# Performance work log

Measured on AMD Instinct MI355X. Metric: run time of the kernel, lower is better.

Reference implementation:

```python
import jax, jax.numpy as jnp
import numpy as np

B, T, DIM = 2, 2048, 2048
H, HKV = 16, 4
D = DIM // H          # head_dim = 128
G = H // HKV          # GQA group = 4
ROPE_BASE = 10000.0
TRAIN_SEQ_LEN = 1024  # Rotary default; T > this triggers NTK base rescale


def _rope_tables():
    # Faithful to Rotary.forward: NTK scaling when seq_len > train_seq_len.
    if T > TRAIN_SEQ_LEN:
        sc = T / TRAIN_SEQ_LEN
        base = ROPE_BASE * sc ** (D / (D - 2))
    else:
        base = ROPE_BASE
    inv = 1.0 / base ** (np.arange(0, D, 2, dtype=np.float32) / D)  # [D/2]
    f = np.outer(np.arange(T, dtype=np.float32), inv)               # [T, D/2]
    cos = jnp.asarray(np.cos(f), jnp.float32)[None, :, None, :]     # [1,T,1,D/2]
    sin = jnp.asarray(np.sin(f), jnp.float32)[None, :, None, :]
    return cos, sin


def _rms_norm(x):
    # F.rms_norm with no weight: x / sqrt(mean(x^2) + eps), eps = finfo(dtype).eps
    eps = jnp.finfo(x.dtype).eps
    return x * jax.lax.rsqrt(jnp.mean(x * x, axis=-1, keepdims=True) + eps)


def _apply_rope(x, cos, sin):
    x1, x2 = jnp.split(x, 2, axis=-1)
    return jnp.concatenate([x1 * cos + x2 * sin, -x1 * sin + x2 * cos], axis=-1)


def setup_inputs() -> dict:
    key = jax.random.key(0)
    kx, kq, kk, kv, kp = jax.random.split(key, 5)
    s = lambda fan_in: 1.0 / np.sqrt(fan_in)
    kv_dim = HKV * D
    return {
        "x": jax.random.normal(kx, (B, T, DIM), jnp.float32),
        "Wq": jax.random.normal(kq, (DIM, DIM), jnp.float32) * s(DIM),
        "Wk": jax.random.normal(kk, (kv_dim, DIM), jnp.float32) * s(DIM),
        "Wv": jax.random.normal(kv, (kv_dim, DIM), jnp.float32) * s(DIM),
        "Wproj": jax.random.normal(kp, (DIM, DIM), jnp.float32) * s(DIM),
        "q_gain": jnp.full((H,), 1.0, jnp.float32),
    }


def reference(x, Wq, Wk, Wv, Wproj, q_gain):
    # QKV projections (bias-free linears)
    q = (x @ Wq.T).reshape(B, T, H, D)
    k = (x @ Wk.T).reshape(B, T, HKV, D)
    v = (x @ Wv.T).reshape(B, T, HKV, D)

    # QK RMSNorm + RoPE + per-head q gain
    q = _rms_norm(q)
    k = _rms_norm(k)
    cos, sin = _rope_tables()
    q = _apply_rope(q, cos, sin)
    k = _apply_rope(k, cos, sin)
    q = q * q_gain[None, None, :, None]

    # GQA causal SDPA without materializing repeated K/V:
    # group query heads by kv head: q -> [B,T,HKV,G,D]
    qg = q.reshape(B, T, HKV, G, D)
    scores = jnp.einsum('btkgd,bskd->bkgts', qg, k) / np.sqrt(D)  # [B,HKV,G,T,T]
    causal = jnp.tril(jnp.ones((T, T), bool))
    scores = jnp.where(causal[None, None, None], scores, -jnp.inf)
    p = jax.nn.softmax(scores, axis=-1)
    y = jnp.einsum('bkgts,bskd->btkgd', p, v).reshape(B, T, H, D)

    out = y.reshape(B, T, DIM) @ Wproj.T
    return out, v
```

## Files before the change

kernel.cpp:

```cpp
#include <hip/hip_runtime.h>
#include <hip/hip_bf16.h>

typedef __bf16 bf16_t;
typedef __bf16 bf16x4 __attribute__((ext_vector_type(4)));
typedef __bf16 bf16x8 __attribute__((ext_vector_type(8)));
typedef float f32x4 __attribute__((ext_vector_type(4)));

#define B_    2
#define T_    2048
#define DIM_  2048
#define H_    16
#define HKV_  4
#define D_    128
#define KVDIM_ 512

__device__ __forceinline__ bf16x8 cvt8(f32x4 a, f32x4 b) {
  bf16x8 r;
  r[0] = (bf16_t)a[0]; r[1] = (bf16_t)a[1]; r[2] = (bf16_t)a[2]; r[3] = (bf16_t)a[3];
  r[4] = (bf16_t)b[0]; r[5] = (bf16_t)b[1]; r[6] = (bf16_t)b[2]; r[7] = (bf16_t)b[3];
  return r;
}
__device__ __forceinline__ bf16x4 cvt4(f32x4 a) {
  bf16x4 r;
  r[0] = (bf16_t)a[0]; r[1] = (bf16_t)a[1]; r[2] = (bf16_t)a[2]; r[3] = (bf16_t)a[3];
  return r;
}
__device__ __forceinline__ void g2l16(const void* g, void* l) {
  __builtin_amdgcn_global_load_lds(
      (const __attribute__((address_space(1))) unsigned int*)g,
      (__attribute__((address_space(3))) unsigned int*)l, 16, 0, 0);
}

__global__ __launch_bounds__(256)
void cvt_all(const float* __restrict__ x,  const float* __restrict__ wq,
             const float* __restrict__ wk, const float* __restrict__ wv,
             const float* __restrict__ wp, bf16_t* __restrict__ xb,
             bf16_t* __restrict__ wqkvb, bf16_t* __restrict__ wpb) {
  int blk = blockIdx.x;
  const float* s; bf16_t* d; int lb;
  if (blk < 4096)      { s = x;  d = xb;                              lb = blk; }
  else if (blk < 6144) { s = wq; d = wqkvb;                           lb = blk - 4096; }
  else if (blk < 6656) { s = wk; d = wqkvb + (size_t)2048 * DIM_;     lb = blk - 6144; }
  else if (blk < 7168) { s = wv; d = wqkvb + (size_t)2560 * DIM_;     lb = blk - 6656; }
  else                 { s = wp; d = wpb;                             lb = blk - 7168; }
  size_t i = (size_t)lb * 2048 + (size_t)threadIdx.x * 8;
  f32x4 a = *(const f32x4*)(s + i);
  f32x4 b = *(const f32x4*)(s + i + 4);
  *(bf16x8*)(d + i) = cvt8(a, b);
}

template <int MODE, bool AASYNC, bool WASYNC>
__global__ __launch_bounds__(256)
void gemm128(const void* __restrict__ Ag, const void* __restrict__ Wg,
             const void* __restrict__ Wg2, void* __restrict__ Cb,
             bf16_t* __restrict__ Kb, bf16_t* __restrict__ Vb,
             float* __restrict__ Vf, int M, int N, int K) {
  constexpr int LDA = AASYNC ? 32 : 40;
  constexpr int LDW = WASYNC ? 32 : 40;
  __shared__ bf16_t As[128 * LDA];
  __shared__ bf16_t Ws[128 * LDW];
  const int tid  = threadIdx.x;
  const int wave = tid >> 6, lane = tid & 63;
  const int l16  = lane & 15, lg = lane >> 4;
  const int m0 = blockIdx.y * 128, n0 = blockIdx.x * 128;
  const int wm = (wave & 1) * 64, wn = (wave >> 1) * 64;
  f32x4 acc[4][4] = {};

  for (int k0 = 0; k0 < K; k0 += 32) {
    __syncthreads();
    if constexpr (AASYNC) {
      const bf16_t* A = (const bf16_t*)Ag;
      const int r = lane >> 2, c8 = (lane & 3) * 8;
      g2l16(&A[(size_t)(m0 + wave * 32 + r) * K + k0 + c8],      &As[(wave * 32) * LDA]);
      g2l16(&A[(size_t)(m0 + wave * 32 + 16 + r) * K + k0 + c8], &As[(wave * 32 + 16) * LDA]);
    } else {
      const float* A = (const float*)Ag;
#pragma unroll
      for (int j = 0; j < 4; j++) {
        int row = wave * 32 + j * 8 + (lane >> 3);
        int cf  = (lane & 7) * 4;
        f32x4 v = *(const f32x4*)&A[(size_t)(m0 + row) * K + k0 + cf];
        *(bf16x4*)&As[row * LDA + cf] = cvt4(v);
      }
    }
    if constexpr (WASYNC) {
      const bf16_t* W = (const bf16_t*)Wg;
      const int r = lane >> 2, c8 = (lane & 3) * 8;
      g2l16(&W[(size_t)(n0 + wave * 32 + r) * K + k0 + c8],      &Ws[(wave * 32) * LDW]);
      g2l16(&W[(size_t)(n0 + wave * 32 + 16 + r) * K + k0 + c8], &Ws[(wave * 32 + 16) * LDW]);
    } else {
      const float* W;
      int nb;
      if constexpr (MODE == 3) {
        if (n0 < 512) { W = (const float*)Wg;  nb = n0; }
        else          { W = (const float*)Wg2; nb = n0 - 512; }
      } else { W = (const float*)Wg; nb = n0; }
#pragma unroll
      for (int j = 0; j < 4; j++) {
        int row = wave * 32 + j * 8 + (lane >> 3);
        int cf  = (lane & 7) * 4;
        f32x4 v = *(const f32x4*)&W[(size_t)(nb + row) * K + k0 + cf];
        *(bf16x4*)&Ws[row * LDW + cf] = cvt4(v);
      }
    }
    __syncthreads();
    bf16x8 af[4], bfr[4];
#pragma unroll
    for (int i = 0; i < 4; i++)
      af[i] = *(const bf16x8*)&As[(wm + i * 16 + l16) * LDA + lg * 8];
#pragma unroll
    for (int j = 0; j < 4; j++)
      bfr[j] = *(const bf16x8*)&Ws[(wn + j * 16 + l16) * LDW + lg * 8];
#pragma unroll
    for (int i = 0; i < 4; i++)
#pragma unroll
      for (int j = 0; j < 4; j++)
        acc[i][j] = __builtin_amdgcn_mfma_f32_16x16x32_bf16(af[i], bfr[j], acc[i][j], 0, 0, 0);
  }
#pragma unroll
  for (int i = 0; i < 4; i++)
#pragma unroll
    for (int j = 0; j < 4; j++) {
      int row = m0 + wm + i * 16 + lg * 4;
      int col = n0 + wn + j * 16 + l16;
#pragma unroll
      for (int r = 0; r < 4; r++) {
        float v = acc[i][j][r];
        if constexpr (MODE == 0) {
          ((bf16_t*)Cb)[(size_t)(row + r) * N + col] = (bf16_t)v;
        } else if constexpr (MODE == 2) {
          ((float*)Cb)[(size_t)(row + r) * N + col] = v;
        } else if constexpr (MODE == 1) {
          if (col < 2048)      ((bf16_t*)Cb)[(size_t)(row + r) * 2048 + col] = (bf16_t)v;
          else if (col < 2560) Kb[(size_t)(row + r) * 512 + (col - 2048)] = (bf16_t)v;
          else {
            int c = col - 2560;
            Vb[(size_t)(row + r) * 512 + c] = (bf16_t)v;
            Vf[(size_t)(row + r) * 512 + c] = v;
          }
        } else {
          if (col < 512) ((bf16_t*)Cb)[(size_t)(row + r) * 512 + col] = (bf16_t)v;
          else {
            int c = col - 512;
            Vb[(size_t)(row + r) * 512 + c] = (bf16_t)v;
            Vf[(size_t)(row + r) * 512 + c] = v;
          }
        }
      }
    }
}

#define SB() __builtin_amdgcn_sched_barrier(0)
#define BARRIER() __builtin_amdgcn_s_barrier()
#define LGKM0() do { asm volatile("s_waitcnt lgkmcnt(0)" ::: "memory"); SB(); } while (0)
#define VMW(N) do { asm volatile("s_waitcnt vmcnt(" #N ")" ::: "memory"); SB(); } while (0)

#define RD_A(BUF, QM) do { \
  _Pragma("unroll") for (int f_ = 0; f_ < 4; f_++) { \
    const int r_ = wm * 128 + (QM) * 64 + f_ * 16 + l16; \
    _Pragma("unroll") for (int ks_ = 0; ks_ < 2; ks_++) \
      a[f_][ks_] = *(const bf16x8*)(lds + (BUF) * 65536 + r_ * 128 + ((ks_ * 64 + lg * 16) ^ swz)); \
  } } while (0)

#define RD_B(BUF, QN, BB) do { \
  _Pragma("unroll") for (int n_ = 0; n_ < 2; n_++) { \
    const int r_ = wn * 64 + (QN) * 32 + n_ * 16 + l16; \
    _Pragma("unroll") for (int ks_ = 0; ks_ < 2; ks_++) \
      BB[n_][ks_] = *(const bf16x8*)(lds + (BUF) * 65536 + 32768 + r_ * 128 + ((ks_ * 64 + lg * 16) ^ swz)); \
  } } while (0)

#define MM(QM, QN, BB) do { \
  __builtin_amdgcn_s_setprio(1); \
  _Pragma("unroll") for (int f_ = 0; f_ < 4; f_++) \
    _Pragma("unroll") for (int n_ = 0; n_ < 2; n_++) \
      _Pragma("unroll") for (int ks_ = 0; ks_ < 2; ks_++) \
        acc[(QM) * 4 + f_][(QN) * 2 + n_] = __builtin_amdgcn_mfma_f32_16x16x32_bf16( \
            a[f_][ks_], BB[n_][ks_], acc[(QM) * 4 + f_][(QN) * 2 + n_], 0, 0, 0); \
  __builtin_amdgcn_s_setprio(0); \
  } while (0)

#define K_ITER(KT0, LAST) do { \
  const int kA1_ = ((KT0) + 1) * 64; \
  const int kN2_ = ((KT0) + 2) * 64; \
  const int kN3_ = ((KT0) + 3) * 64; \
   \
  RD_A(0, 0); RD_B(0, 0, b0); \
  stage_half(Ag, m0, kA1_, 65536); \
  asm volatile("s_waitcnt lgkmcnt(8)" ::: "memory"); \
  SB(); BARRIER(); LGKM0(); \
  MM(0, 0, b0); \
  SB(); BARRIER(); \
   \
  RD_B(0, 1, b1); \
  stage_half(Ag, m0 + 128, kA1_, 65536 + 16384); \
  SB(); BARRIER(); LGKM0(); \
  MM(0, 1, b1); \
  SB(); BARRIER(); \
   \
  RD_A(0, 1); \
  if (!(LAST)) stage_half(Wg, n0, kN2_, 32768); \
  SB(); BARRIER(); LGKM0(); \
  MM(1, 0, b0); \
  SB(); BARRIER(); \
   \
  if (!(LAST)) { stage_half(Wg, n0 + 128, kN2_, 32768 + 16384); VMW(4); } \
  else { VMW(0); } \
  SB(); BARRIER(); \
  MM(1, 1, b1); \
  SB(); BARRIER(); \
   \
  RD_A(1, 0); RD_B(1, 0, b0); \
  if (!(LAST)) stage_half(Ag, m0, kN2_, 0); \
  asm volatile("s_waitcnt lgkmcnt(8)" ::: "memory"); \
  SB(); BARRIER(); LGKM0(); \
  MM(0, 0, b0); \
  SB(); BARRIER(); \
   \
  RD_B(1, 1, b1); \
  if (!(LAST)) stage_half(Ag, m0 + 128, kN2_, 16384); \
  SB(); BARRIER(); LGKM0(); \
  MM(0, 1, b1); \
  SB(); BARRIER(); \
   \
  RD_A(1, 1); \
  if (!(LAST)) stage_half(Wg, n0, kN3_, 65536 + 32768); \
  SB(); BARRIER(); LGKM0(); \
  MM(1, 0, b0); \
  SB(); BARRIER(); \
   \
  if (!(LAST)) { stage_half(Wg, n0 + 128, kN3_, 65536 + 32768 + 16384); VMW(4); } \
  SB(); BARRIER(); \
  MM(1, 1, b1); \
  SB(); BARRIER(); \
} while (0)

template <int MODE>
__global__ __launch_bounds__(512, 2)
void gemm256(const bf16_t* __restrict__ Ag, const bf16_t* __restrict__ Wg,
             void* __restrict__ Cb, bf16_t* __restrict__ Kb, bf16_t* __restrict__ Vb,
             float* __restrict__ Vf, int M, int N, int K) {
  (void)M;
  __shared__ __align__(16) char lds[131072];
  const int tid  = threadIdx.x;
  const int wave = tid >> 6, lane = tid & 63;
  const int l16  = lane & 15, lg = lane >> 4;
  const int wm = wave >> 2, wn = wave & 3;
  const int swz = (l16 & 7) << 4;
  const int m0 = blockIdx.y * 256, n0 = blockIdx.x * 256;
  const int srow = lane >> 3;
  const int scol = ((lane & 7) ^ srow) * 8;

  auto stage_half = [&](const bf16_t* __restrict__ X, int xrow, int k0, int ldsoff) {
    const bf16_t* src = X + (size_t)(xrow + wave * 16 + srow) * K + (k0 + scol);
    char* dst = lds + ldsoff + wave * 2048;
    g2l16(src, dst);
    g2l16(src + (size_t)8 * K, dst + 1024);
  };

  f32x4 acc[8][4] = {};
  bf16x8 a[4][2], b0[2][2], b1[2][2];

  stage_half(Ag, m0,        0, 0);
  stage_half(Ag, m0 + 128,  0, 16384);
  stage_half(Wg, n0,        0, 32768);
  stage_half(Wg, n0 + 128,  0, 32768 + 16384);
  stage_half(Wg, n0,       64, 65536 + 32768);
  stage_half(Wg, n0 + 128, 64, 65536 + 32768 + 16384);
  VMW(4);
  BARRIER();

  const int NIT = K >> 7;
  for (int it = 0; it < NIT - 1; ++it) {
    K_ITER(2 * it, 0);
  }
  K_ITER(2 * (NIT - 1), 1);

#pragma unroll
  for (int mf = 0; mf < 8; mf++)
#pragma unroll
    for (int nf = 0; nf < 4; nf++) {
      const int row = m0 + wm * 128 + mf * 16 + lg * 4;
      const int col = n0 + wn * 64 + nf * 16 + l16;
#pragma unroll
      for (int r = 0; r < 4; r++) {
        float v = acc[mf][nf][r];
        if constexpr (MODE == 1) {
          if (col < 2048)      ((bf16_t*)Cb)[(size_t)(row + r) * 2048 + col] = (bf16_t)v;
          else if (col < 2560) Kb[(size_t)(row + r) * 512 + (col - 2048)] = (bf16_t)v;
          else {
            int c = col - 2560;
            Vb[(size_t)(row + r) * 512 + c] = (bf16_t)v;
            Vf[(size_t)(row + r) * 512 + c] = v;
          }
        } else {
          ((float*)Cb)[(size_t)(row + r) * N + col] = v;
        }
      }
    }
}

__global__ __launch_bounds__(256)
void qk_norm_rope(bf16_t* __restrict__ Qp, bf16_t* __restrict__ Kp,
                  const float* __restrict__ gain) {
  const int lane = threadIdx.x & 63;
  int row = blockIdx.x * 4 + (threadIdx.x >> 6);
  bf16_t* Xp; int nh; bool ag;
  const int MQ = B_ * T_ * H_;
  if (row < MQ) { Xp = Qp; nh = H_;  ag = true; }
  else          { Xp = Kp; nh = HKV_; ag = false; row -= MQ; }
  const int h = row % nh;
  const int t = (row / nh) % T_;
  bf16_t* p = Xp + (size_t)row * D_;
  float x0 = (float)p[lane * 2 + 0];
  float x1 = (float)p[lane * 2 + 1];
  float ss = x0 * x0 + x1 * x1;
#pragma unroll
  for (int m = 32; m >= 1; m >>= 1) ss += __shfl_xor(ss, m);
  const float rn = rsqrtf(ss * (1.0f / 128.0f) + 1.1920929e-07f);
  x0 *= rn; x1 *= rn;
  const float y0 = __shfl_xor(x0, 32);
  const float y1 = __shfl_xor(x1, 32);
  const int i0 = (lane & 31) * 2;
  const float kfreq = -0.22349352180347601f;
  float s0, c0, s1, c1;
  float a0 = (float)t * exp2f(kfreq * (float)i0);
  float a1 = (float)t * exp2f(kfreq * (float)(i0 + 1));
  sincosf(a0, &s0, &c0);
  sincosf(a1, &s1, &c1);
  float o0, o1;
  if (lane < 32) { o0 = x0 * c0 + y0 * s0;  o1 = x1 * c1 + y1 * s1; }
  else           { o0 = x0 * c0 - y0 * s0;  o1 = x1 * c1 - y1 * s1; }
  if (ag) { float g = gain[h]; o0 *= g; o1 *= g; }
  p[lane * 2 + 0] = (bf16_t)o0;
  p[lane * 2 + 1] = (bf16_t)o1;
}

#define KLD 136
#define VLD 72

__global__ __launch_bounds__(256, 2)
void flash_attn(const bf16_t* __restrict__ Q, const bf16_t* __restrict__ Kg,
                const bf16_t* __restrict__ V, bf16_t* __restrict__ Y) {
  __shared__ bf16_t Ks[64 * KLD];
  __shared__ bf16_t Vs[D_ * VLD];
  const int tid  = threadIdx.x;
  const int wave = tid >> 6, lane = tid & 63;
  const int l16  = lane & 15, lg = lane >> 4;
  const int b = blockIdx.z, h = blockIdx.y;
  const int pi = blockIdx.x;
  const int hk = h >> 2;

  int qr[2];
  qr[0] = 64 * pi + 16 * wave;
  qr[1] = 64 * (31 - pi) + 16 * wave;

  bf16x8 qf[2][4];
#pragma unroll
  for (int mt = 0; mt < 2; mt++)
#pragma unroll
    for (int kk = 0; kk < 4; kk++)
      qf[mt][kk] = *(const bf16x8*)&Q[(((size_t)b * T_ + qr[mt] + l16) * H_ + h) * D_ + kk * 32 + lg * 8];

  f32x4 o[2][8] = {};
  float lsum[2] = {};
  const float C = 0.12752531f;

  const int sr = tid >> 4, sc = (tid & 15) * 8;
  const int sp2 = (tid & 31) * 2;
  const int dvh = (tid >> 5) * 8;
  const int ssl = (sp2 & 3) | (((sp2 >> 4) & 1) << 2) | (((sp2 >> 2) & 1) << 3)
                | (((sp2 >> 3) & 1) << 4) | (sp2 & 32);

  bf16x8 kreg[4];
  bf16x8 vreg[2][2];
  auto pf_load = [&](int k0) {
#pragma unroll
    for (int j = 0; j < 4; j++)
      kreg[j] = *(const bf16x8*)&Kg[(((size_t)b * T_ + k0 + sr + 16 * j) * HKV_ + hk) * D_ + sc];
#pragma unroll
    for (int it = 0; it < 2; it++) {
      const bf16_t* vb = &V[(((size_t)b * T_ + k0 + sp2) * HKV_ + hk) * D_ + dvh + it * 64];
      vreg[it][0] = *(const bf16x8*)vb;
      vreg[it][1] = *(const bf16x8*)(vb + HKV_ * D_);
    }
  };
  auto pf_store = [&]() {
#pragma unroll
    for (int j = 0; j < 4; j++)
      *(bf16x8*)&Ks[(sr + 16 * j) * KLD + sc] = kreg[j];
#pragma unroll
    for (int it = 0; it < 2; it++) {
      int dd = dvh + it * 64;
      const unsigned short* au = (const unsigned short*)&vreg[it][0];
      const unsigned short* bu = (const unsigned short*)&vreg[it][1];
#pragma unroll
      for (int i = 0; i < 8; i++) {
        unsigned int pr = (unsigned int)au[i] | ((unsigned int)bu[i] << 16);
        *(unsigned int*)&Vs[(dd + i) * VLD + ssl] = pr;
      }
    }
  };

  const int nkb = 32 - pi;
  pf_load(0);
  for (int kb = 0; kb < nkb; kb++) {
    const int k0 = kb * 64;
    __syncthreads();
    pf_store();
    __syncthreads();
    if (kb + 1 < nkb) pf_load(k0 + 64);

    const bool act0 = (kb <= pi);

    f32x4 s[2][4] = {};
#pragma unroll
    for (int kk = 0; kk < 4; kk++) {
      bf16x8 kf[4];
#pragma unroll
      for (int f = 0; f < 4; f++)
        kf[f] = *(const bf16x8*)&Ks[(f * 16 + l16) * KLD + kk * 32 + lg * 8];
      if (act0)
#pragma unroll
        for (int f = 0; f < 4; f++)
          s[0][f] = __builtin_amdgcn_mfma_f32_16x16x32_bf16(kf[f], qf[0][kk], s[0][f], 0, 0, 0);
#pragma unroll
      for (int f = 0; f < 4; f++)
        s[1][f] = __builtin_amdgcn_mfma_f32_16x16x32_bf16(kf[f], qf[1][kk], s[1][f], 0, 0, 0);
    }
    bf16x8 pfr[2][2];
#pragma unroll
    for (int mt = 0; mt < 2; mt++) {
      if (mt == 0 && !act0) continue;
      const bool diag = (mt == 0) ? (kb == pi) : (kb == nkb - 1);
      const int myq = qr[mt] + l16;
      if (diag) {
#pragma unroll
        for (int f = 0; f < 4; f++)
#pragma unroll
          for (int r = 0; r < 4; r++) {
            int kg = k0 + f * 16 + lg * 4 + r;
            float p = (kg <= myq) ? exp2f(s[mt][f][r] * C) : 0.0f;
            lsum[mt] += p;
            s[mt][f][r] = p;
          }
      } else {
#pragma unroll
        for (int f = 0; f < 4; f++)
#pragma unroll
          for (int r = 0; r < 4; r++) {
            float p = exp2f(s[mt][f][r] * C);
            lsum[mt] += p;
            s[mt][f][r] = p;
          }
      }
      pfr[mt][0] = cvt8(s[mt][0], s[mt][1]);
      pfr[mt][1] = cvt8(s[mt][2], s[mt][3]);
    }
#pragma unroll
    for (int f = 0; f < 8; f++) {
      bf16x8 v0 = *(const bf16x8*)&Vs[(f * 16 + l16) * VLD + lg * 8];
      bf16x8 v1 = *(const bf16x8*)&Vs[(f * 16 + l16) * VLD + 32 + lg * 8];
      if (act0) {
        o[0][f] = __builtin_amdgcn_mfma_f32_16x16x32_bf16(pfr[0][0], v0, o[0][f], 0, 0, 0);
        o[0][f] = __builtin_amdgcn_mfma_f32_16x16x32_bf16(pfr[0][1], v1, o[0][f], 0, 0, 0);
      }
      o[1][f] = __builtin_amdgcn_mfma_f32_16x16x32_bf16(pfr[1][0], v0, o[1][f], 0, 0, 0);
      o[1][f] = __builtin_amdgcn_mfma_f32_16x16x32_bf16(pfr[1][1], v1, o[1][f], 0, 0, 0);
    }
  }
#pragma unroll
  for (int mt = 0; mt < 2; mt++) {
    float l = lsum[mt];
    l += __shfl_xor(l, 16);
    l += __shfl_xor(l, 32);
    const float inv = 1.0f / l;
    float rlv[4];
#pragma unroll
    for (int r = 0; r < 4; r++) rlv[r] = __shfl(inv, lg * 4 + r);
#pragma unroll
    for (int f = 0; f < 8; f++)
#pragma unroll
      for (int r = 0; r < 4; r++) {
        int t = qr[mt] + lg * 4 + r;
        Y[(((size_t)b * T_ + t) * H_ + h) * D_ + f * 16 + l16] = (bf16_t)(o[mt][f][r] * rlv[r]);
      }
  }
}

extern "C" void kernel_launch(void* const* d_in, const int* in_sizes, int n_in,
                              void* d_out, int out_size, void* d_ws, size_t ws_size,
                              hipStream_t stream) {
  (void)in_sizes; (void)n_in; (void)out_size;
  const float* x     = (const float*)d_in[0];
  const float* Wq    = (const float*)d_in[1];
  const float* Wk    = (const float*)d_in[2];
  const float* Wv    = (const float*)d_in[3];
  const float* Wproj = (const float*)d_in[4];
  const float* qgain = (const float*)d_in[5];

  float* out  = (float*)d_out;
  float* vout = out + (size_t)B_ * T_ * DIM_;

  const size_t M = (size_t)B_ * T_;
  char* ws = (char*)d_ws;
  size_t off = 0;
  auto take = [&](size_t elems) { bf16_t* p = (bf16_t*)(ws + off); off += elems * sizeof(bf16_t); return p; };

  bf16_t* Qp = take(M * DIM_);
  bf16_t* Kp = take(M * KVDIM_);
  bf16_t* Vb = take(M * KVDIM_);

  const size_t cvt_elems = M * DIM_ + (size_t)3072 * DIM_ + (size_t)DIM_ * DIM_;
  const bool fast = (ws_size >= off + cvt_elems * sizeof(bf16_t));

  dim3 blk(256);
  if (fast) {
    bf16_t* xb     = take(M * DIM_);
    bf16_t* Wqkvb  = take((size_t)3072 * DIM_);
    bf16_t* Wpb    = take((size_t)DIM_ * DIM_);

    cvt_all<<<dim3(9216), blk, 0, stream>>>(x, Wq, Wk, Wv, Wproj, xb, Wqkvb, Wpb);

    gemm256<1><<<dim3(3072 / 256, M / 256), dim3(512), 0, stream>>>(
        xb, Wqkvb, Qp, Kp, Vb, vout, (int)M, 3072, DIM_);

    qk_norm_rope<<<dim3((unsigned)((M * H_ + M * HKV_) / 4)), blk, 0, stream>>>(Qp, Kp, qgain);
    flash_attn<<<dim3(16, H_, B_), blk, 0, stream>>>(Qp, Kp, Vb, Qp);

    gemm256<2><<<dim3(DIM_ / 256, M / 256), dim3(512), 0, stream>>>(
        Qp, Wpb, out, nullptr, nullptr, nullptr, (int)M, DIM_, DIM_);
  } else {
    gemm128<0, false, false><<<dim3(DIM_ / 128, M / 128), blk, 0, stream>>>(
        x, Wq, nullptr, Qp, nullptr, nullptr, nullptr, M, DIM_, DIM_);
    gemm128<3, false, false><<<dim3(2 * KVDIM_ / 128, M / 128), blk, 0, stream>>>(
        x, Wk, Wv, Kp, nullptr, Vb, vout, M, 2 * KVDIM_, DIM_);
    qk_norm_rope<<<dim3((unsigned)((M * H_ + M * HKV_) / 4)), blk, 0, stream>>>(Qp, Kp, qgain);
    flash_attn<<<dim3(16, H_, B_), blk, 0, stream>>>(Qp, Kp, Vb, Qp);
    gemm128<2, true, false><<<dim3(DIM_ / 128, M / 128), blk, 0, stream>>>(
        Qp, Wproj, nullptr, out, nullptr, nullptr, nullptr, M, DIM_, DIM_);
  }
}
```

Measured before the change: 315.0 us.

## Double-buffer K/V in LDS with direct global-to-LDS K loads and XOR swizzle

Flash attention now keeps two LDS buffers for K and V. The next K tile is staged with direct global-to-LDS loads (g2l16) into an XOR-swizzled layout with no padding, and the V store into the other buffer happens between the QK and PV phases. This leaves one barrier per iteration instead of two, so loads overlap compute. Raising wave priority around the MFMA blocks is also added. Doubling the buffers raises LDS use, which could limit occupancy at 2 blocks per CU.

```diff
diff --git a/kernel.cpp b/kernel.cpp
--- a/kernel.cpp
+++ b/kernel.cpp
@@ -335,14 +335,13 @@
   p[lane * 2 + 1] = (bf16_t)o1;
 }
 
-#define KLD 136
 #define VLD 72
 
 __global__ __launch_bounds__(256, 2)
 void flash_attn(const bf16_t* __restrict__ Q, const bf16_t* __restrict__ Kg,
                 const bf16_t* __restrict__ V, bf16_t* __restrict__ Y) {
-  __shared__ bf16_t Ks[64 * KLD];
-  __shared__ bf16_t Vs[D_ * VLD];
+  __shared__ bf16_t Ks[2][64 * 128];
+  __shared__ bf16_t Vs[2][D_ * VLD];
   const int tid  = threadIdx.x;
   const int wave = tid >> 6, lane = tid & 63;
   const int l16  = lane & 15, lg = lane >> 4;
@@ -365,18 +364,13 @@
   float lsum[2] = {};
   const float C = 0.12752531f;
 
-  const int sr = tid >> 4, sc = (tid & 15) * 8;
   const int sp2 = (tid & 31) * 2;
   const int dvh = (tid >> 5) * 8;
   const int ssl = (sp2 & 3) | (((sp2 >> 4) & 1) << 2) | (((sp2 >> 2) & 1) << 3)
                 | (((sp2 >> 3) & 1) << 4) | (sp2 & 32);
 
-  bf16x8 kreg[4];
   bf16x8 vreg[2][2];
-  auto pf_load = [&](int k0) {
-#pragma unroll
-    for (int j = 0; j < 4; j++)
-      kreg[j] = *(const bf16x8*)&Kg[(((size_t)b * T_ + k0 + sr + 16 * j) * HKV_ + hk) * D_ + sc];
+  auto vload = [&](int k0) {
 #pragma unroll
     for (int it = 0; it < 2; it++) {
       const bf16_t* vb = &V[(((size_t)b * T_ + k0 + sp2) * HKV_ + hk) * D_ + dvh + it * 64];
@@ -384,10 +378,7 @@
       vreg[it][1] = *(const bf16x8*)(vb + HKV_ * D_);
     }
   };
-  auto pf_store = [&]() {
-#pragma unroll
-    for (int j = 0; j < 4; j++)
-      *(bf16x8*)&Ks[(sr + 16 * j) * KLD + sc] = kreg[j];
+  auto vstore = [&](int buf) {
 #pragma unroll
     for (int it = 0; it < 2; it++) {
       int dd = dvh + it * 64;
@@ -396,19 +387,34 @@
 #pragma unroll
       for (int i = 0; i < 8; i++) {
         unsigned int pr = (unsigned int)au[i] | ((unsigned int)bu[i] << 16);
-        *(unsigned int*)&Vs[(dd + i) * VLD + ssl] = pr;
+        *(unsigned int*)&Vs[buf][(dd + i) * VLD + ssl] = pr;
       }
     }
   };
+  auto kstage = [&](int buf, int k0) {
+#pragma unroll
+    for (int j = 0; j < 4; j++) {
+      const int rbase = wave * 16 + j * 4;
+      const int row = rbase + (lane >> 4);
+      const int cf = ((lane & 15) ^ (row & 7)) * 8;
+      g2l16(&Kg[(((size_t)b * T_ + k0 + row) * HKV_ + hk) * D_ + cf],
+            (char*)&Ks[buf][0] + rbase * 256);
+    }
+  };
 
   const int nkb = 32 - pi;
-  pf_load(0);
+  kstage(0, 0);
+  vload(0);
+  VMW(0);
+  vstore(0);
+  LGKM0();
+  BARRIER();
+
   for (int kb = 0; kb < nkb; kb++) {
     const int k0 = kb * 64;
-    __syncthreads();
-    pf_store();
-    __syncthreads();
-    if (kb + 1 < nkb) pf_load(k0 + 64);
+    const int cur = kb & 1, nxt = cur ^ 1;
+    const bool more = (kb + 1 < nkb);
+    if (more) { kstage(nxt, k0 + 64); vload(k0 + 64); }
 
     const bool act0 = (kb <= pi);
 
@@ -418,7 +424,9 @@
       bf16x8 kf[4];
 #pragma unroll
       for (int f = 0; f < 4; f++)
-        kf[f] = *(const bf16x8*)&Ks[(f * 16 + l16) * KLD + kk * 32 + lg * 8];
+        kf[f] = *(const bf16x8*)((const char*)&Ks[cur][0] + (f * 16 + l16) * 256
+                                 + ((kk * 64 + lg * 16) ^ ((l16 & 7) << 4)));
+      __builtin_amdgcn_s_setprio(1);
       if (act0)
 #pragma unroll
         for (int f = 0; f < 4; f++)
@@ -426,6 +434,7 @@
 #pragma unroll
       for (int f = 0; f < 4; f++)
         s[1][f] = __builtin_amdgcn_mfma_f32_16x16x32_bf16(kf[f], qf[1][kk], s[1][f], 0, 0, 0);
+      __builtin_amdgcn_s_setprio(0);
     }
     bf16x8 pfr[2][2];
 #pragma unroll
@@ -456,16 +465,24 @@
       pfr[mt][0] = cvt8(s[mt][0], s[mt][1]);
       pfr[mt][1] = cvt8(s[mt][2], s[mt][3]);
     }
+    if (more) vstore(nxt);
 #pragma unroll
     for (int f = 0; f < 8; f++) {
-      bf16x8 v0 = *(const bf16x8*)&Vs[(f * 16 + l16) * VLD + lg * 8];
-      bf16x8 v1 = *(const bf16x8*)&Vs[(f * 16 + l16) * VLD + 32 + lg * 8];
+      bf16x8 v0 = *(const bf16x8*)&Vs[cur][(f * 16 + l16) * VLD + lg * 8];
+      bf16x8 v1 = *(const bf16x8*)&Vs[cur][(f * 16 + l16) * VLD + 32 + lg * 8];
+      __builtin_amdgcn_s_setprio(1);
       if (act0) {
         o[0][f] = __builtin_amdgcn_mfma_f32_16x16x32_bf16(pfr[0][0], v0, o[0][f], 0, 0, 0);
         o[0][f] = __builtin_amdgcn_mfma_f32_16x16x32_bf16(pfr[0][1], v1, o[0][f], 0, 0, 0);
       }
       o[1][f] = __builtin_amdgcn_mfma_f32_16x16x32_bf16(pfr[1][0], v0, o[1][f], 0, 0, 0);
       o[1][f] = __builtin_amdgcn_mfma_f32_16x16x32_bf16(pfr[1][1], v1, o[1][f], 0, 0, 0);
+      __builtin_amdgcn_s_setprio(0);
+    }
+    if (more) {
+      VMW(0);
+      LGKM0();
+      BARRIER();
     }
   }
 #pragma unroll
```

Result: slower. 323.2 us (+2.6%).
